# Kernel tuning notes

Measured on AMD Instinct MI355X. Metric: run time of the kernel, lower is better.

## Reference

```python
import jax, jax.numpy as jnp
import numpy as np

N, D = 8192, 128

def setup_inputs() -> dict:
    key = jax.random.key(0)
    kF, kS = jax.random.split(key)
    F = jax.random.normal(kF, (N, D), dtype=jnp.float32)
    S = jax.random.uniform(kS, (N, N), dtype=jnp.float32)
    return {"F": F, "S": S, "t": 1, "T": 10}

def reference(F, S, t, T):
    # Pairwise squared euclidean distances via Gram trick:
    # D_ij = ||f_i||^2 + ||f_j||^2 - 2 f_i . f_j  (same math as norm(F[:,None]-F)^2)
    sq = jnp.sum(F * F, axis=1)                      # [N]
    dist2 = sq[:, None] + sq[None, :] - 2.0 * (F @ F.T)  # [N, N]
    # select=False: loss = sum over i of sum_j dist2[i,j] * S[i,j]
    loss = jnp.sum(dist2 * S)
    return loss
```

## Files before the change

### kernel.cpp

```cpp
#include <hip/hip_runtime.h>

#define NN 8192
#define DD 128
#define BM 128
#define NTILE (NN / BM)

typedef __attribute__((ext_vector_type(8))) short bf16x8;
typedef __attribute__((ext_vector_type(4))) float f32x4;

__device__ __forceinline__ ushort f2bf(float x) {
    unsigned u = __float_as_uint(x);
    unsigned r = u + 0x7FFFu + ((u >> 16) & 1u);
    return (ushort)(r >> 16);
}

__device__ __forceinline__ void async16(void* lds, const void* g) {
    __builtin_amdgcn_global_load_lds(
        (const __attribute__((address_space(1))) unsigned*)g,
        (__attribute__((address_space(3))) unsigned*)lds, 16, 0, 0);
}
__device__ __forceinline__ void async4(void* lds, const void* g) {
    __builtin_amdgcn_global_load_lds(
        (const __attribute__((address_space(1))) unsigned*)g,
        (__attribute__((address_space(3))) unsigned*)lds, 4, 0, 0);
}

__global__ void prep_kernel(const float* __restrict__ F, ushort* __restrict__ Fbf,
                            float* __restrict__ sq, int doFbf) {
    int gtid = blockIdx.x * blockDim.x + threadIdx.x;
    int row  = gtid >> 6;
    int lane = threadIdx.x & 63;
    const float2 v = *(const float2*)(F + (size_t)row * DD + lane * 2);
    if (doFbf)
        ((ushort2*)(Fbf + (size_t)row * DD))[lane] = make_ushort2(f2bf(v.x), f2bf(v.y));
    float s = v.x * v.x + v.y * v.y;
    #pragma unroll
    for (int off = 32; off > 0; off >>= 1) s += __shfl_down(s, off);
    if (lane == 0) sq[row] = s;
}

__global__ __launch_bounds__(512, 4) void tile_kernel(
        const ushort* __restrict__ Fbf, const float* __restrict__ S,
        const float* __restrict__ sq, float* __restrict__ partials) {
    __shared__ ushort lI[BM * DD];
    __shared__ ushort lJ[BM * DD];
    __shared__ float  sqi[BM];
    __shared__ float  sqj[BM];
    __shared__ float  red[8];

    const int gi = blockIdx.y * BM, gj = blockIdx.x * BM;
    const int tid = threadIdx.x;
    const int w = tid >> 6, l = tid & 63;

    #pragma unroll
    for (int it = 0; it < 4; ++it) {
        const int chunk = it * 8 + w;
        const int row = chunk * 4 + (l >> 4);
        const int src = ((l & 15) * 16) ^ ((row & 7) << 4);
        async16((char*)lI + chunk * 1024, (const char*)(Fbf + (size_t)(gi + row) * DD) + src);
        async16((char*)lJ + chunk * 1024, (const char*)(Fbf + (size_t)(gj + row) * DD) + src);
    }
    if (w < 4) {
        float* dstb = (w < 2 ? sqi : sqj) + (w & 1) * 64;
        const float* srcb = sq + (w < 2 ? gi : gj) + (w & 1) * 64 + l;
        async4(dstb, srcb);
    }
    __syncthreads();

    const int fr = l & 15;
    const int g  = l >> 4;
    const int jw = w * 16;

    f32x4 sv[8];
    const float* sb = S + (size_t)(gi + fr) * NN + gj + jw + g * 4;
    #pragma unroll
    for (int ct = 0; ct < 8; ++ct)
        sv[ct] = *(const f32x4*)(sb + (size_t)ct * 16 * NN);
    __builtin_amdgcn_sched_barrier(0);

    bf16x8 afrag[4];
    #pragma unroll
    for (int kk = 0; kk < 4; ++kk) {
        const int row = jw + fr;
        int byte = row * 256 + kk * 64 + g * 16;
        byte ^= (row & 7) << 4;
        afrag[kk] = *(const bf16x8*)((const char*)lJ + byte);
    }

    f32x4 acc[8];
    #pragma unroll
    for (int ct = 0; ct < 8; ++ct) acc[ct] = (f32x4){0.f, 0.f, 0.f, 0.f};

    #pragma unroll
    for (int ct = 0; ct < 8; ++ct) {
        const int row = ct * 16 + fr;
        const int sw  = (row & 7) << 4;
        #pragma unroll
        for (int kk = 0; kk < 4; ++kk) {
            const bf16x8 bfrag = *(const bf16x8*)((const char*)lI + row * 256 +
                                                  ((kk * 64 + g * 16) ^ sw));
            acc[ct] = __builtin_amdgcn_mfma_f32_16x16x32_bf16(afrag[kk], bfrag, acc[ct], 0, 0, 0);
        }
    }

    const float4 sjv = *(const float4*)(sqj + jw + g * 4);
    float part0 = 0.f, part1 = 0.f;
    #pragma unroll
    for (int ct = 0; ct < 8; ++ct) {
        const float sic = sqi[ct * 16 + fr];
        const f32x4 s4 = sv[ct];
        part0 += s4.x * ((sic + sjv.x) - 2.f * acc[ct][0]);
        part1 += s4.y * ((sic + sjv.y) - 2.f * acc[ct][1]);
        part0 += s4.z * ((sic + sjv.z) - 2.f * acc[ct][2]);
        part1 += s4.w * ((sic + sjv.w) - 2.f * acc[ct][3]);
    }
    float part = part0 + part1;

    #pragma unroll
    for (int off = 32; off > 0; off >>= 1) part += __shfl_down(part, off);
    if (l == 0) red[w] = part;
    __syncthreads();
    if (tid == 0)
        partials[blockIdx.y * gridDim.x + blockIdx.x] =
            ((red[0] + red[1]) + (red[2] + red[3])) +
            ((red[4] + red[5]) + (red[6] + red[7]));
}

__global__ __launch_bounds__(256, 2) void tile_fb_kernel(
        const float* __restrict__ F, const float* __restrict__ S,
        const float* __restrict__ sq, float* __restrict__ partials) {
    __shared__ ushort lI[BM * DD];
    __shared__ ushort lJ[BM * DD];
    __shared__ float  sqi[BM];
    __shared__ float  sqj[BM];
    __shared__ float  red[4];

    const int gi = blockIdx.y * BM, gj = blockIdx.x * BM;
    const int tid = threadIdx.x;
    const int w = tid >> 6, l = tid & 63;

    const int r0 = tid >> 5;
    const int c4 = (tid & 31) * 4;
    #pragma unroll
    for (int it = 0; it < 16; ++it) {
        const int row = it * 8 + r0;
        const float4 va = *(const float4*)(F + (size_t)(gi + row) * DD + c4);
        const float4 vb = *(const float4*)(F + (size_t)(gj + row) * DD + c4);
        int byte = row * 256 + c4 * 2;
        byte ^= (row & 7) << 4;
        *(ushort4*)((char*)lI + byte) =
            make_ushort4(f2bf(va.x), f2bf(va.y), f2bf(va.z), f2bf(va.w));
        *(ushort4*)((char*)lJ + byte) =
            make_ushort4(f2bf(vb.x), f2bf(vb.y), f2bf(vb.z), f2bf(vb.w));
    }
    if (tid < 128) sqi[tid] = sq[gi + tid];
    else           sqj[tid - 128] = sq[gj + tid - 128];
    __syncthreads();

    const int fr = l & 15;
    const int g  = l >> 4;
    const int jw = w * 32;

    float4 sv0[8], sv1[8];
    #pragma unroll
    for (int ct = 0; ct < 8; ++ct) {
        const float* srow = S + (size_t)(gi + ct * 16 + fr) * NN + gj + jw + g * 4;
        sv0[ct] = *(const float4*)(srow);
        sv1[ct] = *(const float4*)(srow + 16);
    }

    bf16x8 afrag[2][4];
    #pragma unroll
    for (int kk = 0; kk < 4; ++kk) {
        int row = jw + fr;
        int byte = row * 256 + kk * 64 + g * 16; byte ^= (row & 7) << 4;
        afrag[0][kk] = *(const bf16x8*)((const char*)lJ + byte);
        row = jw + 16 + fr;
        byte = row * 256 + kk * 64 + g * 16; byte ^= (row & 7) << 4;
        afrag[1][kk] = *(const bf16x8*)((const char*)lJ + byte);
    }

    f32x4 acc[2][8];
    #pragma unroll
    for (int ct = 0; ct < 8; ++ct) {
        acc[0][ct] = (f32x4){0.f, 0.f, 0.f, 0.f};
        acc[1][ct] = (f32x4){0.f, 0.f, 0.f, 0.f};
    }
    #pragma unroll
    for (int ct = 0; ct < 8; ++ct) {
        #pragma unroll
        for (int kk = 0; kk < 4; ++kk) {
            const int row = ct * 16 + fr;
            int byte = row * 256 + kk * 64 + g * 16; byte ^= (row & 7) << 4;
            const bf16x8 bfrag = *(const bf16x8*)((const char*)lI + byte);
            acc[0][ct] = __builtin_amdgcn_mfma_f32_16x16x32_bf16(afrag[0][kk], bfrag, acc[0][ct], 0, 0, 0);
            acc[1][ct] = __builtin_amdgcn_mfma_f32_16x16x32_bf16(afrag[1][kk], bfrag, acc[1][ct], 0, 0, 0);
        }
    }

    const float4 sj0 = *(const float4*)(sqj + jw + g * 4);
    const float4 sj1 = *(const float4*)(sqj + jw + 16 + g * 4);
    float part = 0.f;
    #pragma unroll
    for (int ct = 0; ct < 8; ++ct) {
        const float sic = sqi[ct * 16 + fr];
        const float4 s0 = sv0[ct], s1 = sv1[ct];
        part += s0.x * (sic + sj0.x - 2.f * acc[0][ct][0]);
        part += s0.y * (sic + sj0.y - 2.f * acc[0][ct][1]);
        part += s0.z * (sic + sj0.z - 2.f * acc[0][ct][2]);
        part += s0.w * (sic + sj0.w - 2.f * acc[0][ct][3]);
        part += s1.x * (sic + sj1.x - 2.f * acc[1][ct][0]);
        part += s1.y * (sic + sj1.y - 2.f * acc[1][ct][1]);
        part += s1.z * (sic + sj1.z - 2.f * acc[1][ct][2]);
        part += s1.w * (sic + sj1.w - 2.f * acc[1][ct][3]);
    }

    #pragma unroll
    for (int off = 32; off > 0; off >>= 1) part += __shfl_down(part, off);
    if (l == 0) red[w] = part;
    __syncthreads();
    if (tid == 0)
        partials[blockIdx.y * gridDim.x + blockIdx.x] = (red[0] + red[1]) + (red[2] + red[3]);
}

__global__ void reduce_kernel(const float* __restrict__ partials, float* __restrict__ out) {
    __shared__ float sm[256];
    const int t = threadIdx.x;
    float s = 0.f;
    for (int i = t; i < NTILE * NTILE; i += 256) s += partials[i];
    sm[t] = s;
    __syncthreads();
    for (int off = 128; off > 0; off >>= 1) {
        if (t < off) sm[t] += sm[t + off];
        __syncthreads();
    }
    if (t == 0) out[0] = sm[0];
}

extern "C" void kernel_launch(void* const* d_in, const int* in_sizes, int n_in,
                              void* d_out, int out_size, void* d_ws, size_t ws_size,
                              hipStream_t stream) {
    const float* F = (const float*)d_in[0];
    const float* S = (const float*)d_in[1];
    float* sq       = (float*)d_ws;
    float* partials = sq + NN;
    ushort* Fbf     = (ushort*)((char*)d_ws + 48 * 1024);
    float* out      = (float*)d_out;

    const size_t need = 48 * 1024 + (size_t)NN * DD * 2 + 256;
    const int fast = (ws_size >= need) ? 1 : 0;

    prep_kernel<<<NN / 4, 256, 0, stream>>>(F, Fbf, sq, fast);
    dim3 grid(NTILE, NTILE);
    if (fast)
        tile_kernel<<<grid, 512, 0, stream>>>(Fbf, S, sq, partials);
    else
        tile_fb_kernel<<<grid, 256, 0, stream>>>(F, S, sq, partials);
    reduce_kernel<<<1, 256, 0, stream>>>(partials, out);
}
```

Baseline: 63.93 us.

## Double tile_kernel block to 1024 threads, splitting column tiles across wave halves

The tile kernel now launches 1024 threads (16 waves) per 128x128 tile instead of 512. Each wave handles half as many 16-row column tiles (4 instead of 8), and the async LDS load loop and the final block reduction are adjusted to match. The aim is more memory-level parallelism on the S stream and lower per-thread register pressure. The cost is more LDS pressure per CU, since 64KB per block limits residency, and a larger block-level sync and reduction.

```diff
diff --git a/kernel.cpp b/kernel.cpp
--- a/kernel.cpp
+++ b/kernel.cpp
@@ -39,22 +39,26 @@
     if (lane == 0) sq[row] = s;
 }
 
-__global__ __launch_bounds__(512, 4) void tile_kernel(
+__global__ __launch_bounds__(1024, 8) void tile_kernel(
         const ushort* __restrict__ Fbf, const float* __restrict__ S,
         const float* __restrict__ sq, float* __restrict__ partials) {
     __shared__ ushort lI[BM * DD];
     __shared__ ushort lJ[BM * DD];
     __shared__ float  sqi[BM];
     __shared__ float  sqj[BM];
-    __shared__ float  red[8];
+    __shared__ float  red[16];
 
     const int gi = blockIdx.y * BM, gj = blockIdx.x * BM;
     const int tid = threadIdx.x;
     const int w = tid >> 6, l = tid & 63;
-
-    #pragma unroll
-    for (int it = 0; it < 4; ++it) {
-        const int chunk = it * 8 + w;
+    const int fr = l & 15;
+    const int g  = l >> 4;
+    const int jw  = (w & 7) * 16;
+    const int ct0 = (w >> 3) * 4;
+
+    #pragma unroll
+    for (int it = 0; it < 2; ++it) {
+        const int chunk = it * 16 + w;
         const int row = chunk * 4 + (l >> 4);
         const int src = ((l & 15) * 16) ^ ((row & 7) << 4);
         async16((char*)lI + chunk * 1024, (const char*)(Fbf + (size_t)(gi + row) * DD) + src);
@@ -67,52 +71,49 @@
     }
     __syncthreads();
 
-    const int fr = l & 15;
-    const int g  = l >> 4;
-    const int jw = w * 16;
-
-    f32x4 sv[8];
-    const float* sb = S + (size_t)(gi + fr) * NN + gj + jw + g * 4;
-    #pragma unroll
-    for (int ct = 0; ct < 8; ++ct)
-        sv[ct] = *(const f32x4*)(sb + (size_t)ct * 16 * NN);
+    f32x4 sv[4];
+    #pragma unroll
+    for (int c = 0; c < 4; ++c)
+        sv[c] = *(const f32x4*)(S + (size_t)(gi + (ct0 + c) * 16 + fr) * NN +
+                                gj + jw + g * 4);
     __builtin_amdgcn_sched_barrier(0);
 
     bf16x8 afrag[4];
-    #pragma unroll
-    for (int kk = 0; kk < 4; ++kk) {
+    {
         const int row = jw + fr;
-        int byte = row * 256 + kk * 64 + g * 16;
-        byte ^= (row & 7) << 4;
-        afrag[kk] = *(const bf16x8*)((const char*)lJ + byte);
-    }
-
-    f32x4 acc[8];
-    #pragma unroll
-    for (int ct = 0; ct < 8; ++ct) acc[ct] = (f32x4){0.f, 0.f, 0.f, 0.f};
-
-    #pragma unroll
-    for (int ct = 0; ct < 8; ++ct) {
-        const int row = ct * 16 + fr;
+        const int sw  = (row & 7) << 4;
+        #pragma unroll
+        for (int kk = 0; kk < 4; ++kk)
+            afrag[kk] = *(const bf16x8*)((const char*)lJ + row * 256 +
+                                         ((kk * 64 + g * 16) ^ sw));
+    }
+
+    f32x4 acc[4];
+    #pragma unroll
+    for (int c = 0; c < 4; ++c) acc[c] = (f32x4){0.f, 0.f, 0.f, 0.f};
+
+    #pragma unroll
+    for (int c = 0; c < 4; ++c) {
+        const int row = (ct0 + c) * 16 + fr;
         const int sw  = (row & 7) << 4;
         #pragma unroll
         for (int kk = 0; kk < 4; ++kk) {
             const bf16x8 bfrag = *(const bf16x8*)((const char*)lI + row * 256 +
                                                   ((kk * 64 + g * 16) ^ sw));
-            acc[ct] = __builtin_amdgcn_mfma_f32_16x16x32_bf16(afrag[kk], bfrag, acc[ct], 0, 0, 0);
+            acc[c] = __builtin_amdgcn_mfma_f32_16x16x32_bf16(afrag[kk], bfrag, acc[c], 0, 0, 0);
         }
     }
 
     const float4 sjv = *(const float4*)(sqj + jw + g * 4);
     float part0 = 0.f, part1 = 0.f;
     #pragma unroll
-    for (int ct = 0; ct < 8; ++ct) {
-        const float sic = sqi[ct * 16 + fr];
-        const f32x4 s4 = sv[ct];
-        part0 += s4.x * ((sic + sjv.x) - 2.f * acc[ct][0]);
-        part1 += s4.y * ((sic + sjv.y) - 2.f * acc[ct][1]);
-        part0 += s4.z * ((sic + sjv.z) - 2.f * acc[ct][2]);
-        part1 += s4.w * ((sic + sjv.w) - 2.f * acc[ct][3]);
+    for (int c = 0; c < 4; ++c) {
+        const float sic = sqi[(ct0 + c) * 16 + fr];
+        const f32x4 s4 = sv[c];
+        part0 += s4.x * ((sic + sjv.x) - 2.f * acc[c][0]);
+        part1 += s4.y * ((sic + sjv.y) - 2.f * acc[c][1]);
+        part0 += s4.z * ((sic + sjv.z) - 2.f * acc[c][2]);
+        part1 += s4.w * ((sic + sjv.w) - 2.f * acc[c][3]);
     }
     float part = part0 + part1;
 
@@ -120,10 +121,12 @@
     for (int off = 32; off > 0; off >>= 1) part += __shfl_down(part, off);
     if (l == 0) red[w] = part;
     __syncthreads();
-    if (tid == 0)
-        partials[blockIdx.y * gridDim.x + blockIdx.x] =
-            ((red[0] + red[1]) + (red[2] + red[3])) +
-            ((red[4] + red[5]) + (red[6] + red[7]));
+    if (tid == 0) {
+        float r = 0.f;
+        #pragma unroll
+        for (int k = 0; k < 16; ++k) r += red[k];
+        partials[blockIdx.y * gridDim.x + blockIdx.x] = r;
+    }
 }
 
 __global__ __launch_bounds__(256, 2) void tile_fb_kernel(
@@ -253,7 +256,7 @@
     prep_kernel<<<NN / 4, 256, 0, stream>>>(F, Fbf, sq, fast);
     dim3 grid(NTILE, NTILE);
     if (fast)
-        tile_kernel<<<grid, 512, 0, stream>>>(Fbf, S, sq, partials);
+        tile_kernel<<<grid, 1024, 0, stream>>>(Fbf, S, sq, partials);
     else
         tile_fb_kernel<<<grid, 256, 0, stream>>>(F, S, sq, partials);
     reduce_kernel<<<1, 256, 0, stream>>>(partials, out);
```

After: 64.72 us. No clear change (+1.2%).
